# Optimization experiments

Hardware: AMD Instinct MI355X
Metric: run time of the kernel (lower is better)

The kernel has to match this reference:

```python
import jax, jax.numpy as jnp
import numpy as np
import math

NUM_HEADS = 16
CONSTITUENCY_PENALTY = 0.5
CONSTITUENT_BLOCK = 64  # deterministic stand-in for the ChomskyParser constituency spans


def constituency_penalty_mask(seq_len, dtype):
    # Tokens in the same constituent (contiguous block) attend freely;
    # cross-constituent pairs are penalized by CONSTITUENCY_PENALTY.
    blk = jnp.arange(seq_len) // CONSTITUENT_BLOCK
    return jnp.where(blk[:, None] != blk[None, :], CONSTITUENCY_PENALTY, 0.0).astype(dtype)


def setup_inputs() -> dict:
    key = jax.random.key(0)
    ks = jax.random.split(key, 7)
    B, S, H = 8, 1024, 1024
    scale = 1.0 / math.sqrt(H)
    return {
        "hidden_states": jax.random.normal(ks[0], (B, S, H), jnp.float32),
        "Wq": jax.random.normal(ks[1], (H, H), jnp.float32) * scale,
        "bq": jnp.zeros((H,), jnp.float32),
        "Wk": jax.random.normal(ks[2], (H, H), jnp.float32) * scale,
        "bk": jnp.zeros((H,), jnp.float32),
        "Wv": jax.random.normal(ks[3], (H, H), jnp.float32) * scale,
        "bv": jnp.zeros((H,), jnp.float32),
    }


def reference(hidden_states, Wq, bq, Wk, bk, Wv, bv):
    B, S, H = hidden_states.shape
    nh = NUM_HEADS
    hd = H // nh

    def heads(x):  # [B,S,H] -> [B,nh,S,hd]
        return x.reshape(B, S, nh, hd).transpose(0, 2, 1, 3)

    q = heads(hidden_states @ Wq + bq)
    k = heads(hidden_states @ Wk + bk)
    v = heads(hidden_states @ Wv + bv)

    scores = jnp.einsum("bhqd,bhkd->bhqk", q, k) / jnp.sqrt(jnp.asarray(hd, q.dtype))
    # constituency penalty subtracted before softmax (broadcast over batch, heads)
    scores = scores - constituency_penalty_mask(S, scores.dtype)[None, None, :, :]
    probs = jax.nn.softmax(scores, axis=-1)  # dropout is identity in eval

    ctx = jnp.einsum("bhqk,bhkd->bhqd", probs, v)
    ctx = ctx.transpose(0, 2, 1, 3).reshape(B, S, H)
    return ctx
```

## Files before the change

kernel.cpp:

```cpp
#include <hip/hip_runtime.h>
#include <cstdint>

#define BB 8
#define SQ 1024
#define HH 1024
#define NH 16
#define HD 64

typedef __attribute__((ext_vector_type(4))) float f32x4;
typedef __attribute__((ext_vector_type(16))) float f32x16;
typedef __attribute__((ext_vector_type(8))) __bf16 bf16x8;
typedef __attribute__((ext_vector_type(8))) unsigned short u16x8;
typedef __attribute__((ext_vector_type(4))) unsigned short u16x4;
typedef __attribute__((ext_vector_type(4))) unsigned int u32x4;

__device__ __forceinline__ unsigned short f2bf(float f){
  uint32_t u = __builtin_bit_cast(uint32_t, f);
  u += 0x7FFFu + ((u >> 16) & 1u);
  return (unsigned short)(u >> 16);
}

__device__ __forceinline__ void gload_lds16(const void* g, void* l){
  __builtin_amdgcn_global_load_lds((__attribute__((address_space(1))) void*)g,
                                   (__attribute__((address_space(3))) void*)l,
                                   16, 0, 0);
}

__global__ __launch_bounds__(256) void k_prep(const float* __restrict__ x,
                                              unsigned short* __restrict__ xb,
                                              const float* __restrict__ Wq,
                                              const float* __restrict__ Wk,
                                              const float* __restrict__ Wv,
                                              unsigned short* __restrict__ wt){
  __shared__ float t[32][33];
  int bid = blockIdx.x, tid = threadIdx.x;
  if(bid < 4096){
    int i = bid * 256 + tid;
    const f32x4* xv = (const f32x4*)x;
    f32x4 a = xv[2*i], b = xv[2*i+1];
    u16x8 o;
    o[0]=f2bf(a[0]); o[1]=f2bf(a[1]); o[2]=f2bf(a[2]); o[3]=f2bf(a[3]);
    o[4]=f2bf(b[0]); o[5]=f2bf(b[1]); o[6]=f2bf(b[2]); o[7]=f2bf(b[3]);
    ((u16x8*)xb)[i] = o;
  } else {
    int idx = bid - 4096;
    int p = idx >> 10, rem = idx & 1023;
    const float* W = (p==0)?Wq:((p==1)?Wk:Wv);
    int n0 = (rem & 31)*32, k0 = (rem >> 5)*32;
    int tx = tid & 31, ty = tid >> 5;
    #pragma unroll
    for(int j=0;j<32;j+=8) t[ty+j][tx] = W[(size_t)(k0+ty+j)*HH + n0+tx];
    __syncthreads();
    unsigned short* o = wt + (size_t)p*HH*HH;
    #pragma unroll
    for(int j=0;j<32;j+=8) o[(size_t)(n0+ty+j)*HH + k0+tx] = f2bf(t[tx][ty+j]);
  }
}

#define BM 128
#define BN 128
#define BK 64
__global__ __launch_bounds__(256) void k_qkv(const unsigned short* __restrict__ Xb,
                                             const unsigned short* __restrict__ Wt,
                                             const float* __restrict__ bq,
                                             const float* __restrict__ bk,
                                             const float* __restrict__ bv,
                                             unsigned short* __restrict__ q_ws,
                                             unsigned short* __restrict__ k_ws,
                                             unsigned short* __restrict__ vt_ws){
  __shared__ __align__(16) unsigned short As[BM*BK];
  __shared__ __align__(16) unsigned short Bs[BN*BK];
  int tid = threadIdx.x;
  int lane = tid & 63, wid = tid >> 6;
  int nt = blockIdx.x % 24, mt = blockIdx.x / 24;
  int m0 = mt*BM, n0 = nt*BN;
  int wm = (wid & 1)*64, wn = (wid >> 1)*64;
  int lr = lane & 15, g = lane >> 4;

  const f32x4 zf = {0.f,0.f,0.f,0.f};
  f32x4 acc[4][4];
  #pragma unroll
  for(int a=0;a<4;a++)
    #pragma unroll
    for(int b=0;b<4;b++) acc[a][b] = zf;

  for(int kk=0; kk<1024; kk+=BK){
    __syncthreads();
    #pragma unroll
    for(int it=0; it<4; it++){
      int slot = it*256 + tid;
      int row = slot >> 3, ch = (slot & 7) ^ (row & 7);
      gload_lds16(Xb + (size_t)(m0+row)*1024 + kk + ch*8, &As[slot*8]);
    }
    #pragma unroll
    for(int it=0; it<4; it++){
      int slot = it*256 + tid;
      int row = slot >> 3, ch = (slot & 7) ^ (row & 7);
      gload_lds16(Wt + (size_t)(n0+row)*1024 + kk + ch*8, &Bs[slot*8]);
    }
    __syncthreads();

    #pragma unroll
    for(int ks=0; ks<2; ks++){
      bf16x8 af[4], bfr[4];
      #pragma unroll
      for(int mi=0;mi<4;mi++){
        int r = wm + mi*16 + lr;
        af[mi] = *(const bf16x8*)&As[r*64 + (((ks*4+g) ^ (r&7))<<3)];
      }
      #pragma unroll
      for(int ni=0;ni<4;ni++){
        int r = wn + ni*16 + lr;
        bfr[ni] = *(const bf16x8*)&Bs[r*64 + (((ks*4+g) ^ (r&7))<<3)];
      }
      #pragma unroll
      for(int mi=0;mi<4;mi++)
        #pragma unroll
        for(int ni=0;ni<4;ni++)
          acc[mi][ni] = __builtin_amdgcn_mfma_f32_16x16x32_bf16(af[mi], bfr[ni], acc[mi][ni], 0,0,0);
    }
  }

  int proj = n0 >> 10;
  const float* bias = (proj==0)?bq:((proj==1)?bk:bv);
  const float QSCALE = 0.18033688f;
  #pragma unroll
  for(int mi=0;mi<4;mi++){
    #pragma unroll
    for(int ni=0;ni<4;ni++){
      int ncol = n0 + wn + ni*16 + lr;
      int hcol = ncol & 1023;
      int h = hcol >> 6, d = hcol & 63;
      float bval = bias[hcol];
      if(proj == 0){
        #pragma unroll
        for(int i=0;i<4;i++){
          int m = m0 + wm + mi*16 + g*4 + i;
          int b = m >> 10, s = m & 1023;
          q_ws[((size_t)(b*NH + h)*SQ + s)*HD + d] = f2bf((acc[mi][ni][i] + bval)*QSCALE);
        }
      } else if(proj == 1){
        #pragma unroll
        for(int i=0;i<4;i++){
          int m = m0 + wm + mi*16 + g*4 + i;
          int b = m >> 10, s = m & 1023;
          k_ws[((size_t)(b*NH + h)*SQ + s)*HD + d] = f2bf(acc[mi][ni][i] + bval);
        }
      } else {
        int m = m0 + wm + mi*16 + g*4;
        int b = m >> 10, s = m & 1023;
        u16x4 pk;
        #pragma unroll
        for(int i=0;i<4;i++) pk[i] = f2bf(acc[mi][ni][i] + bval);
        *(u16x4*)&vt_ws[((size_t)(b*NH + h)*HD + d)*SQ + s] = pk;
      }
    }
  }
}

__global__ __launch_bounds__(512, 4) void k_attn(const unsigned short* __restrict__ q_ws,
                                                 const unsigned short* __restrict__ k_ws,
                                                 const unsigned short* __restrict__ vt_ws,
                                                 float* __restrict__ out){
  __shared__ __align__(16) unsigned short Ks[2][64*64];
  __shared__ __align__(16) unsigned short Vs[2][64*64];
  int tid = threadIdx.x, lane = tid & 63, wid = tid >> 6;
  int lq = lane & 31, h5 = lane >> 5;
  int bid = blockIdx.x;
  int swz = (bid & 7)*64 + (bid >> 3);
  int qb = swz & 3, bh = swz >> 2;
  int qw = qb*256 + wid*32;
  const unsigned short* qp = q_ws + (size_t)bh*SQ*HD;
  const unsigned short* kp = k_ws + (size_t)bh*SQ*HD;
  const unsigned short* vp = vt_ws + (size_t)bh*HD*SQ;

  bf16x8 qf[4];
  #pragma unroll
  for(int dk=0;dk<4;dk++)
    qf[dk] = *(const bf16x8*)&qp[(size_t)(qw + lq)*HD + dk*16 + h5*8];

  int diag = qw >> 6;

  int srow = tid >> 3;
  int sch  = (tid & 7) ^ (srow & 7);

  f32x16 co[2];
  #pragma unroll
  for(int db=0;db<2;db++)
    #pragma unroll
    for(int r=0;r<16;r++) co[db][r] = 0.f;
  float lacc = 0.f;

  gload_lds16(kp + (size_t)srow*HD + sch*8, &Ks[0][tid*8]);
  gload_lds16(vp + (size_t)srow*SQ + sch*8, &Vs[0][tid*8]);
  __syncthreads();

  int cur = 0;
  for(int kt=0; kt<16; kt++){
    if(kt < 15){
      int kb = (kt+1)*64;
      gload_lds16(kp + (size_t)(kb+srow)*HD + sch*8, &Ks[cur^1][tid*8]);
      gload_lds16(vp + (size_t)srow*SQ + kb + sch*8, &Vs[cur^1][tid*8]);
    }
    float add = (kt == diag) ? 0.72134752f : 0.0f;

    #pragma unroll
    for(int tb=0; tb<2; tb++){
      f32x16 sc;
      #pragma unroll
      for(int r=0;r<16;r++) sc[r] = 0.f;
      int r0 = tb*32 + lq;
      #pragma unroll
      for(int dk=0;dk<4;dk++){
        bf16x8 kf = *(const bf16x8*)&Ks[cur][r0*64 + (((2*dk + h5) ^ (r0&7))<<3)];
        sc = __builtin_amdgcn_mfma_f32_32x32x16_bf16(kf, qf[dk], sc, 0,0,0);
      }
      unsigned int pk[8];
      #pragma unroll
      for(int w=0;w<8;w++){
        float lo = __builtin_amdgcn_exp2f(sc[2*w] + add);
        float hi = __builtin_amdgcn_exp2f(sc[2*w+1] + add);
        lacc += lo + hi;
        pk[w] = (unsigned int)f2bf(lo) | ((unsigned int)f2bf(hi) << 16);
      }
      asm volatile("v_permlane32_swap_b32 %0, %1" : "+v"(pk[0]), "+v"(pk[2]));
      asm volatile("v_permlane32_swap_b32 %0, %1" : "+v"(pk[1]), "+v"(pk[3]));
      asm volatile("v_permlane32_swap_b32 %0, %1" : "+v"(pk[4]), "+v"(pk[6]));
      asm volatile("v_permlane32_swap_b32 %0, %1" : "+v"(pk[5]), "+v"(pk[7]));
      u32x4 w0 = {pk[0], pk[1], pk[2], pk[3]};
      u32x4 w1 = {pk[4], pk[5], pk[6], pk[7]};
      bf16x8 pf0 = __builtin_bit_cast(bf16x8, w0);
      bf16x8 pf1 = __builtin_bit_cast(bf16x8, w1);

      #pragma unroll
      for(int db=0;db<2;db++){
        int vr = db*32 + lq;
        bf16x8 vf0 = *(const bf16x8*)&Vs[cur][vr*64 + (((4*tb + h5) ^ (vr&7))<<3)];
        co[db] = __builtin_amdgcn_mfma_f32_32x32x16_bf16(vf0, pf0, co[db], 0,0,0);
        bf16x8 vf1 = *(const bf16x8*)&Vs[cur][vr*64 + (((4*tb + 2 + h5) ^ (vr&7))<<3)];
        co[db] = __builtin_amdgcn_mfma_f32_32x32x16_bf16(vf1, pf1, co[db], 0,0,0);
      }
    }

    __syncthreads();
    cur ^= 1;
  }

  lacc += __shfl_xor(lacc, 32);
  float rl = 1.0f / lacc;

  int b = bh >> 4, h = bh & 15;
  size_t obase = ((size_t)(b*SQ + qw + lq))*HH + h*HD;
  #pragma unroll
  for(int db=0;db<2;db++){
    #pragma unroll
    for(int w=0;w<4;w++){
      f32x4 r;
      r[0] = co[db][4*w  ] * rl;
      r[1] = co[db][4*w+1] * rl;
      r[2] = co[db][4*w+2] * rl;
      r[3] = co[db][4*w+3] * rl;
      *(f32x4*)&out[obase + db*32 + 8*w + 4*h5] = r;
    }
  }
}

extern "C" void kernel_launch(void* const* d_in, const int* in_sizes, int n_in,
                              void* d_out, int out_size, void* d_ws, size_t ws_size,
                              hipStream_t stream){
  const float* hs = (const float*)d_in[0];
  const float* Wq = (const float*)d_in[1];
  const float* bq = (const float*)d_in[2];
  const float* Wk = (const float*)d_in[3];
  const float* bk = (const float*)d_in[4];
  const float* Wv = (const float*)d_in[5];
  const float* bv = (const float*)d_in[6];
  float* out = (float*)d_out;

  unsigned char* ws = (unsigned char*)d_ws;
  const size_t NX = (size_t)8192*1024;
  unsigned short* xb    = (unsigned short*)ws;
  unsigned short* wt    = (unsigned short*)(ws + NX*2);
  unsigned short* q_ws  = (unsigned short*)(ws + NX*2 + (size_t)3*1024*1024*2);
  unsigned short* k_ws  = q_ws + NX;
  unsigned short* vt_ws = k_ws + NX;

  k_prep<<<7168, 256, 0, stream>>>(hs, xb, Wq, Wk, Wv, wt);
  k_qkv<<<24*64, 256, 0, stream>>>(xb, wt, bq, bk, bv, q_ws, k_ws, vt_ws);
  k_attn<<<512, 512, 0, stream>>>(q_ws, k_ws, vt_ws, out);
}
```

Before: 219.1 us.

## Restructure QKV GEMM with 256x128 tiles, double-buffered LDS and interleaved prefetch

The QKV projection GEMM goes from 128x128 tiles with 256 threads and a single LDS buffer to 256x128 tiles with 512 threads (8 waves) and double-buffered LDS. Loads for the next K-tile are split into chunks issued between MFMA phases, with explicit vmcnt waits, barriers and s_setprio raised around the MFMA bursts. It also swizzles the block order for L2 locality. The goal is to hide global-to-LDS latency behind matrix math and raise arithmetic intensity. The cost is doubled LDS use (96KB per block), fewer blocks in flight, and fragile manual wait counts.

```diff
diff --git a/kernel.cpp b/kernel.cpp
--- a/kernel.cpp
+++ b/kernel.cpp
@@ -57,101 +57,165 @@
   }
 }
 
-#define BM 128
-#define BN 128
-#define BK 64
-__global__ __launch_bounds__(256) void k_qkv(const unsigned short* __restrict__ Xb,
-                                             const unsigned short* __restrict__ Wt,
-                                             const float* __restrict__ bq,
-                                             const float* __restrict__ bk,
-                                             const float* __restrict__ bv,
-                                             unsigned short* __restrict__ q_ws,
-                                             unsigned short* __restrict__ k_ws,
-                                             unsigned short* __restrict__ vt_ws){
-  __shared__ __align__(16) unsigned short As[BM*BK];
-  __shared__ __align__(16) unsigned short Bs[BN*BK];
+#define QBM 256
+#define QBN 128
+#define QBK 64
+__global__ __launch_bounds__(512, 2) void k_qkv(const unsigned short* __restrict__ Xb,
+                                                const unsigned short* __restrict__ Wt,
+                                                const float* __restrict__ bq,
+                                                const float* __restrict__ bk,
+                                                const float* __restrict__ bv,
+                                                unsigned short* __restrict__ q_ws,
+                                                unsigned short* __restrict__ k_ws,
+                                                unsigned short* __restrict__ vt_ws){
+  __shared__ __align__(16) unsigned short As[2][QBM*QBK];
+  __shared__ __align__(16) unsigned short Bs[2][QBN*QBK];
   int tid = threadIdx.x;
   int lane = tid & 63, wid = tid >> 6;
-  int nt = blockIdx.x % 24, mt = blockIdx.x / 24;
-  int m0 = mt*BM, n0 = nt*BN;
-  int wm = (wid & 1)*64, wn = (wid >> 1)*64;
+  int wr = wid >> 2, wc = wid & 3;
+  int bid = blockIdx.x;
+  int sw = (bid & 7)*96 + (bid >> 3);
+  int nt = sw % 24, mt = sw / 24;
+  int m0 = mt*QBM, n0 = nt*QBN;
   int lr = lane & 15, g = lane >> 4;
+  int srow = tid >> 3;
+  int sch  = (tid & 7) ^ (srow & 7);
 
   const f32x4 zf = {0.f,0.f,0.f,0.f};
-  f32x4 acc[4][4];
-  #pragma unroll
-  for(int a=0;a<4;a++)
-    #pragma unroll
-    for(int b=0;b<4;b++) acc[a][b] = zf;
-
-  for(int kk=0; kk<1024; kk+=BK){
-    __syncthreads();
-    #pragma unroll
-    for(int it=0; it<4; it++){
-      int slot = it*256 + tid;
-      int row = slot >> 3, ch = (slot & 7) ^ (row & 7);
-      gload_lds16(Xb + (size_t)(m0+row)*1024 + kk + ch*8, &As[slot*8]);
-    }
-    #pragma unroll
-    for(int it=0; it<4; it++){
-      int slot = it*256 + tid;
-      int row = slot >> 3, ch = (slot & 7) ^ (row & 7);
-      gload_lds16(Wt + (size_t)(n0+row)*1024 + kk + ch*8, &Bs[slot*8]);
-    }
-    __syncthreads();
-
-    #pragma unroll
-    for(int ks=0; ks<2; ks++){
-      bf16x8 af[4], bfr[4];
-      #pragma unroll
-      for(int mi=0;mi<4;mi++){
-        int r = wm + mi*16 + lr;
-        af[mi] = *(const bf16x8*)&As[r*64 + (((ks*4+g) ^ (r&7))<<3)];
-      }
-      #pragma unroll
-      for(int ni=0;ni<4;ni++){
-        int r = wn + ni*16 + lr;
-        bfr[ni] = *(const bf16x8*)&Bs[r*64 + (((ks*4+g) ^ (r&7))<<3)];
-      }
-      #pragma unroll
-      for(int mi=0;mi<4;mi++)
-        #pragma unroll
-        for(int ni=0;ni<4;ni++)
-          acc[mi][ni] = __builtin_amdgcn_mfma_f32_16x16x32_bf16(af[mi], bfr[ni], acc[mi][ni], 0,0,0);
-    }
-  }
+  f32x4 acc[8][2];
+  #pragma unroll
+  for(int a=0;a<8;a++){ acc[a][0] = zf; acc[a][1] = zf; }
+
+  #define ST_A(buf, kb, u, it) gload_lds16( \
+      Xb + (size_t)(m0 + (u)*128 + (it)*64 + srow)*1024 + (kb) + sch*8, \
+      &As[buf][(((u)*2+(it))*512 + tid)*8])
+  #define ST_B(buf, kb, h) gload_lds16( \
+      Wt + (size_t)(n0 + (h)*64 + srow)*1024 + (kb) + sch*8, \
+      &Bs[buf][((h)*512 + tid)*8])
+
+  ST_A(0,0,0,0); ST_A(0,0,0,1); ST_A(0,0,1,0); ST_A(0,0,1,1);
+  ST_B(0,0,0);   ST_B(0,0,1);
+  ST_A(1,QBK,0,0); ST_A(1,QBK,0,1);
+  asm volatile("s_waitcnt vmcnt(2)" ::: "memory");
+  __builtin_amdgcn_s_barrier();
+
+  for(int kt=0; kt<16; kt++){
+    int cur = kt & 1, nxt = cur ^ 1;
+    const unsigned short* Ab = As[cur];
+    const unsigned short* Bb = Bs[cur];
+    int kb1 = (kt+1)*QBK, kb2 = (kt+2)*QBK;
+    bf16x8 bfr[2], af[4];
+
+    #pragma unroll
+    for(int ni=0;ni<2;ni++){
+      int r = wc*32 + ni*16 + lr;
+      bfr[ni] = *(const bf16x8*)&Bb[r*64 + ((g ^ (r&7))<<3)];
+    }
+    #pragma unroll
+    for(int mi=0;mi<4;mi++){
+      int r = wr*128 + mi*16 + lr;
+      af[mi] = *(const bf16x8*)&Ab[r*64 + ((g ^ (r&7))<<3)];
+    }
+    if(kt < 15){ ST_A(nxt,kb1,1,0); ST_A(nxt,kb1,1,1); }
+    __builtin_amdgcn_s_barrier();
+    __builtin_amdgcn_s_setprio(1);
+    #pragma unroll
+    for(int mi=0;mi<4;mi++)
+      #pragma unroll
+      for(int ni=0;ni<2;ni++)
+        acc[mi][ni] = __builtin_amdgcn_mfma_f32_16x16x32_bf16(af[mi], bfr[ni], acc[mi][ni], 0,0,0);
+    __builtin_amdgcn_s_setprio(0);
+    __builtin_amdgcn_s_barrier();
+
+    #pragma unroll
+    for(int mi=0;mi<4;mi++){
+      int r = wr*128 + (4+mi)*16 + lr;
+      af[mi] = *(const bf16x8*)&Ab[r*64 + ((g ^ (r&7))<<3)];
+    }
+    if(kt < 15){ ST_B(nxt,kb1,0); }
+    __builtin_amdgcn_s_barrier();
+    __builtin_amdgcn_s_setprio(1);
+    #pragma unroll
+    for(int mi=0;mi<4;mi++)
+      #pragma unroll
+      for(int ni=0;ni<2;ni++)
+        acc[4+mi][ni] = __builtin_amdgcn_mfma_f32_16x16x32_bf16(af[mi], bfr[ni], acc[4+mi][ni], 0,0,0);
+    __builtin_amdgcn_s_setprio(0);
+    __builtin_amdgcn_s_barrier();
+
+    #pragma unroll
+    for(int ni=0;ni<2;ni++){
+      int r = wc*32 + ni*16 + lr;
+      bfr[ni] = *(const bf16x8*)&Bb[r*64 + (((4+g) ^ (r&7))<<3)];
+    }
+    #pragma unroll
+    for(int mi=0;mi<4;mi++){
+      int r = wr*128 + mi*16 + lr;
+      af[mi] = *(const bf16x8*)&Ab[r*64 + (((4+g) ^ (r&7))<<3)];
+    }
+    if(kt < 15){ ST_B(nxt,kb1,1); }
+    __builtin_amdgcn_s_barrier();
+    __builtin_amdgcn_s_setprio(1);
+    #pragma unroll
+    for(int mi=0;mi<4;mi++)
+      #pragma unroll
+      for(int ni=0;ni<2;ni++)
+        acc[mi][ni] = __builtin_amdgcn_mfma_f32_16x16x32_bf16(af[mi], bfr[ni], acc[mi][ni], 0,0,0);
+    __builtin_amdgcn_s_setprio(0);
+    __builtin_amdgcn_s_barrier();
+
+    #pragma unroll
+    for(int mi=0;mi<4;mi++){
+      int r = wr*128 + (4+mi)*16 + lr;
+      af[mi] = *(const bf16x8*)&Ab[r*64 + (((4+g) ^ (r&7))<<3)];
+    }
+    if(kt < 14){ ST_A(cur,kb2,0,0); ST_A(cur,kb2,0,1); }
+    __builtin_amdgcn_s_barrier();
+    __builtin_amdgcn_s_setprio(1);
+    #pragma unroll
+    for(int mi=0;mi<4;mi++)
+      #pragma unroll
+      for(int ni=0;ni<2;ni++)
+        acc[4+mi][ni] = __builtin_amdgcn_mfma_f32_16x16x32_bf16(af[mi], bfr[ni], acc[4+mi][ni], 0,0,0);
+    __builtin_amdgcn_s_setprio(0);
+    if(kt < 14)       asm volatile("s_waitcnt vmcnt(2)" ::: "memory");
+    else if(kt == 14) asm volatile("s_waitcnt vmcnt(0)" ::: "memory");
+    __builtin_amdgcn_s_barrier();
+  }
+  #undef ST_A
+  #undef ST_B
 
   int proj = n0 >> 10;
   const float* bias = (proj==0)?bq:((proj==1)?bk:bv);
   const float QSCALE = 0.18033688f;
   #pragma unroll
-  for(int mi=0;mi<4;mi++){
-    #pragma unroll
-    for(int ni=0;ni<4;ni++){
-      int ncol = n0 + wn + ni*16 + lr;
+  for(int j=0;j<8;j++){
+    #pragma unroll
+    for(int ni=0;ni<2;ni++){
+      int ncol = n0 + wc*32 + ni*16 + lr;
       int hcol = ncol & 1023;
       int h = hcol >> 6, d = hcol & 63;
       float bval = bias[hcol];
       if(proj == 0){
         #pragma unroll
         for(int i=0;i<4;i++){
-          int m = m0 + wm + mi*16 + g*4 + i;
+          int m = m0 + wr*128 + j*16 + g*4 + i;
           int b = m >> 10, s = m & 1023;
-          q_ws[((size_t)(b*NH + h)*SQ + s)*HD + d] = f2bf((acc[mi][ni][i] + bval)*QSCALE);
+          q_ws[((size_t)(b*NH + h)*SQ + s)*HD + d] = f2bf((acc[j][ni][i] + bval)*QSCALE);
         }
       } else if(proj == 1){
         #pragma unroll
         for(int i=0;i<4;i++){
-          int m = m0 + wm + mi*16 + g*4 + i;
+          int m = m0 + wr*128 + j*16 + g*4 + i;
           int b = m >> 10, s = m & 1023;
-          k_ws[((size_t)(b*NH + h)*SQ + s)*HD + d] = f2bf(acc[mi][ni][i] + bval);
+          k_ws[((size_t)(b*NH + h)*SQ + s)*HD + d] = f2bf(acc[j][ni][i] + bval);
         }
       } else {
-        int m = m0 + wm + mi*16 + g*4;
+        int m = m0 + wr*128 + j*16 + g*4;
         int b = m >> 10, s = m & 1023;
         u16x4 pk;
         #pragma unroll
-        for(int i=0;i<4;i++) pk[i] = f2bf(acc[mi][ni][i] + bval);
+        for(int i=0;i<4;i++) pk[i] = f2bf(acc[j][ni][i] + bval);
         *(u16x4*)&vt_ws[((size_t)(b*NH + h)*HD + d)*SQ + s] = pk;
       }
     }
@@ -286,6 +350,6 @@
   unsigned short* vt_ws = k_ws + NX;
 
   k_prep<<<7168, 256, 0, stream>>>(hs, xb, Wq, Wk, Wv, wt);
-  k_qkv<<<24*64, 256, 0, stream>>>(xb, wt, bq, bk, bv, q_ws, k_ws, vt_ws);
+  k_qkv<<<768, 512, 0, stream>>>(xb, wt, bq, bk, bv, q_ws, k_ws, vt_ws);
   k_attn<<<512, 512, 0, stream>>>(q_ws, k_ws, vt_ws, out);
 }
```

New measurement: 227.1 us. 1.04x slower.
